# Optimization experiments

Hardware: AMD Instinct MI355X
Metric: run time of the kernel (lower is better)

## Reference

```python
import jax, jax.numpy as jnp
import numpy as np
from jax.scipy.linalg import solve_triangular

REG = 1e-6  # reg_covar added to covariance diagonal
LOG2PI = float(np.log(2.0 * np.pi))
RESP_EPS = 10.0 * float(np.finfo(np.float32).eps)


def _log_gauss(X, means, covs):
    # X: [N,D], means: [K,D], covs: [K,D,D] -> per-sample per-component log N(x|mu_k, Sigma_k): [N,K]
    K, D = means.shape
    eye = jnp.eye(D, dtype=X.dtype)
    chol = jnp.linalg.cholesky(covs + REG * eye)                      # [K,D,D]
    diff = X[None, :, :] - means[:, None, :]                          # [K,N,D]
    sol = jax.vmap(lambda L, d: solve_triangular(L, d.T, lower=True))(chol, diff)  # [K,D,N]
    maha = jnp.sum(sol * sol, axis=1)                                 # [K,N]
    logdet = jnp.sum(jnp.log(jnp.diagonal(chol, axis1=1, axis2=2)), axis=1)  # [K] = 0.5*log|Sigma|
    return (-0.5 * (D * LOG2PI + maha) - logdet[:, None]).T           # [N,K]


def _em_step(X, weights, means, covs):
    N, D = X.shape
    # E-step: responsibilities via stable logsumexp
    lp = _log_gauss(X, means, covs) + jnp.log(weights)[None, :]       # [N,K]
    log_norm = jax.scipy.special.logsumexp(lp, axis=1)                # [N]
    resp = jnp.exp(lp - log_norm[:, None])                            # [N,K]
    # M-step (MLE)
    nk = resp.sum(axis=0) + RESP_EPS                                  # [K]
    new_w = nk / N
    new_means = (resp.T @ X) / nk[:, None]                            # [K,D]
    diff = X[None, :, :] - new_means[:, None, :]                      # [K,N,D]
    new_covs = jnp.einsum('kn,knd,kne->kde', resp.T, diff, diff) / nk[:, None, None]
    new_covs = new_covs + REG * jnp.eye(D, dtype=X.dtype)
    return new_w, new_means, new_covs


def reference(X, weights, means, covariances, n_iter):
    # Normalize provided weights (uniform init in the torch module)
    w0 = weights / jnp.sum(weights)

    def step(carry, _):
        w, m, c = carry
        return _em_step(X, w, m, c), None

    (w, m, c), _ = jax.lax.scan(step, (w0, means, covariances), xs=None, length=n_iter)
    # Final per-sample log-likelihood under the fitted mixture (lower bound)
    lp = _log_gauss(X, m, c) + jnp.log(w)[None, :]
    return jax.scipy.special.logsumexp(lp, axis=1)                    # [N]


def setup_inputs() -> dict:
    key = jax.random.key(0)
    kx, km = jax.random.split(key)
    N, D, K = 100000, 32, 16
    X = jax.random.normal(kx, (N, D), dtype=jnp.float32)
    weights = jnp.ones((K,), dtype=jnp.float32) / K
    means = jax.random.normal(km, (K, D), dtype=jnp.float32)
    covariances = jnp.tile(jnp.eye(D, dtype=jnp.float32)[None], (K, 1, 1))
    return {"X": X, "weights": weights, "means": means, "covariances": covariances, "n_iter": 5}
```

## Files before the change

kernel.cpp:

```cpp
#include <hip/hip_runtime.h>
#include <math.h>

#define REGC 1e-6f
#define LOG2PI 1.83787706640934534f
#define RESP_EPS 1.1920929e-6f

#define NPART_MAX 256
#define PART_K 1156
#define PART_BLK (16 * PART_K)
#define RS 16

typedef __attribute__((ext_vector_type(8))) short short8;
typedef __attribute__((ext_vector_type(4))) float f32x4;
typedef unsigned short ushort_t;
typedef unsigned int uint_t;

__device__ __forceinline__ ushort_t f2bf(float x) {
    uint_t u = __float_as_uint(x);
    uint_t r = (u + 0x7fffu + ((u >> 16) & 1u)) >> 16;
    return (ushort_t)r;
}
__device__ __forceinline__ float bf2f(ushort_t h) {
    return __uint_as_float(((uint_t)h) << 16);
}
__device__ __forceinline__ void split2(float av, ushort_t& h, ushort_t& l) {
    uint_t u = __float_as_uint(av);
    float hf = __uint_as_float(u & 0xffff0000u);
    h = (ushort_t)(u >> 16);
    l = f2bf(av - hf);
}

__global__ void gmm_init(const float* __restrict__ w, const float* __restrict__ mu,
                         const float* __restrict__ cov, float* __restrict__ P0) {
    int t = blockIdx.x * 256 + threadIdx.x;
    if (t < 16) {
        float s = 0.f;
        for (int i = 0; i < 16; ++i) s += w[i];
        P0[t] = w[t] / s;
    } else if (t < 528) {
        P0[t] = mu[t - 16];
    } else if (t < 16912) {
        P0[t] = cov[t - 528];
    }
}

__global__ __launch_bounds__(256) void gmm_xsplit(const float* __restrict__ X,
                                                  ushort_t* __restrict__ Xh,
                                                  ushort_t* __restrict__ Xl,
                                                  ushort_t* __restrict__ XTH,
                                                  ushort_t* __restrict__ XTL,
                                                  int N) {
    int chunk = blockIdx.x;
    int t = threadIdx.x;
    __shared__ float xsh[32][33];
    int s = t >> 3, q = t & 7;
    int n = chunk * 32 + s;
    float4 v = make_float4(0.f, 0.f, 0.f, 0.f);
    if (n < N) v = ((const float4*)(X + (size_t)n * 32))[q];
    float vv[4] = { v.x, v.y, v.z, v.w };
    xsh[s][q * 4 + 0] = v.x; xsh[s][q * 4 + 1] = v.y;
    xsh[s][q * 4 + 2] = v.z; xsh[s][q * 4 + 3] = v.w;
    if (n < N) {
        ushort_t h[4], l[4];
#pragma unroll
        for (int i = 0; i < 4; ++i) {
            h[i] = f2bf(vv[i]);
            l[i] = f2bf(vv[i] - bf2f(h[i]));
        }
        size_t o = (size_t)n * 32 + q * 4;
        uint2 hp = make_uint2((uint_t)h[0] | ((uint_t)h[1] << 16),
                              (uint_t)h[2] | ((uint_t)h[3] << 16));
        uint2 lp = make_uint2((uint_t)l[0] | ((uint_t)l[1] << 16),
                              (uint_t)l[2] | ((uint_t)l[3] << 16));
        *(uint2*)(Xh + o) = hp;
        *(uint2*)(Xl + o) = lp;
    }
    __syncthreads();
    int di = t >> 7;
    int lane = (t >> 1) & 63;
    int jj0 = (t & 1) * 4;
    int c = lane & 15, quad = lane >> 4;
    int d = di * 16 + c;
    ushort_t fh[4], fl[4];
#pragma unroll
    for (int i = 0; i < 4; ++i) {
        float x = xsh[quad * 8 + jj0 + i][d];
        fh[i] = f2bf(x);
        fl[i] = f2bf(x - bf2f(fh[i]));
    }
    size_t fo = ((size_t)(chunk * 2 + di) * 64 + lane) * 8 + jj0;
    uint2 hp = make_uint2((uint_t)fh[0] | ((uint_t)fh[1] << 16),
                          (uint_t)fh[2] | ((uint_t)fh[3] << 16));
    uint2 lp = make_uint2((uint_t)fl[0] | ((uint_t)fl[1] << 16),
                          (uint_t)fl[2] | ((uint_t)fl[3] << 16));
    *(uint2*)(XTH + fo) = hp;
    *(uint2*)(XTL + fo) = lp;
}

__global__ __launch_bounds__(64) void gmm_prep(const float* __restrict__ P,
                                               ushort_t* __restrict__ Wh,
                                               ushort_t* __restrict__ Wl,
                                               float* __restrict__ Bv,
                                               float* __restrict__ Cc) {
    int k = blockIdx.x;
    int t = threadIdx.x;
    __shared__ float L[32][33];
    __shared__ float Ai[32][33];
    const float* cov = P + 528 + k * 1024;
    const float* mu  = P + 16 + k * 32;

#pragma unroll
    for (int rep = 0; rep < 16; ++rep) {
        int idx = rep * 64 + t;
        int i = idx >> 5, j = idx & 31;
        L[i][j] = cov[idx] + (i == j ? REGC : 0.f);
    }
    __syncthreads();

#pragma unroll
    for (int j = 0; j < 32; ++j) {
        float s = L[j][j];
#pragma unroll
        for (int p = 0; p < j; ++p) { float v = L[j][p]; s -= v * v; }
        float dj = sqrtf(s);
        if (t > j && t < 32) {
            float s2 = L[t][j];
#pragma unroll
            for (int p = 0; p < j; ++p) s2 -= L[t][p] * L[j][p];
            L[t][j] = s2 / dj;
        }
        if (t == j) L[j][j] = dj;
        __syncthreads();
    }

    if (t < 32) {
        float ai[32];
#pragma unroll
        for (int r = 0; r < 32; ++r) {
            float s = (r == t) ? 1.f : 0.f;
#pragma unroll
            for (int p = 0; p < r; ++p) s -= L[r][p] * ai[p];
            ai[r] = s / L[r][r];
        }
#pragma unroll
        for (int r = 0; r < 32; ++r) Ai[r][t] = ai[r];
    }
    __syncthreads();

#pragma unroll
    for (int rep = 0; rep < 16; ++rep) {
        int idx = rep * 64 + t;
        int i = idx >> 5, j = idx & 31;
        float v = Ai[i][j];
        ushort_t h = f2bf(v);
        Wh[(size_t)(k * 32 + i) * 32 + j] = h;
        Wl[(size_t)(k * 32 + i) * 32 + j] = f2bf(v - bf2f(h));
    }
    if (t < 32) {
        float s = 0.f;
#pragma unroll
        for (int j = 0; j < 32; ++j) s += Ai[t][j] * mu[j];
        Bv[k * 32 + t] = s;
    }
    float lv = (t < 32) ? logf(L[t & 31][t & 31]) : 0.f;
#pragma unroll
    for (int off = 1; off < 32; off <<= 1) lv += __shfl_xor(lv, off);
    if (t == 0) Cc[k] = logf(P[k]) - 0.5f * 32.0f * LOG2PI - lv;
}

__global__ __launch_bounds__(256, 2) void gmm_estep(const ushort_t* __restrict__ Xh,
                                                    const ushort_t* __restrict__ Xl,
                                                    const ushort_t* __restrict__ Wh,
                                                    const ushort_t* __restrict__ Wl,
                                                    const float* __restrict__ Bv,
                                                    const float* __restrict__ Cc,
                                                    float* __restrict__ resp,
                                                    float* __restrict__ out,
                                                    int N, int mode) {
    int t = threadIdx.x;
    int wave = t >> 6, lane = t & 63;
    int quad = lane >> 4, c = lane & 15;
    int base = (blockIdx.x * 4 + wave) * 16;
    if (base + 16 > N) base = (N >= 16) ? (N - 16) : 0;

    short8 ah = *(const short8*)(Xh + (size_t)(base + c) * 32 + quad * 8);
    short8 al = *(const short8*)(Xl + (size_t)(base + c) * 32 + quad * 8);

    f32x4 lpv[16];
#pragma unroll
    for (int k = 0; k < 16; ++k) {
        const size_t w0 = (size_t)(k * 32 + c) * 32 + quad * 8;
        const size_t w1 = (size_t)(k * 32 + 16 + c) * 32 + quad * 8;
        short8 bh0 = *(const short8*)(Wh + w0);
        short8 bl0 = *(const short8*)(Wl + w0);
        short8 bh1 = *(const short8*)(Wh + w1);
        short8 bl1 = *(const short8*)(Wl + w1);
        f32x4 acc0 = {0.f, 0.f, 0.f, 0.f};
        f32x4 acc1 = {0.f, 0.f, 0.f, 0.f};
        acc0 = __builtin_amdgcn_mfma_f32_16x16x32_bf16(ah, bh0, acc0, 0, 0, 0);
        acc0 = __builtin_amdgcn_mfma_f32_16x16x32_bf16(ah, bl0, acc0, 0, 0, 0);
        acc0 = __builtin_amdgcn_mfma_f32_16x16x32_bf16(al, bh0, acc0, 0, 0, 0);
        acc1 = __builtin_amdgcn_mfma_f32_16x16x32_bf16(ah, bh1, acc1, 0, 0, 0);
        acc1 = __builtin_amdgcn_mfma_f32_16x16x32_bf16(ah, bl1, acc1, 0, 0, 0);
        acc1 = __builtin_amdgcn_mfma_f32_16x16x32_bf16(al, bh1, acc1, 0, 0, 0);

        float bv0 = Bv[k * 32 + c];
        float bv1 = Bv[k * 32 + 16 + c];
        f32x4 ms;
#pragma unroll
        for (int r = 0; r < 4; ++r) {
            float d0 = acc0[r] - bv0;
            float d1 = acc1[r] - bv1;
            ms[r] = fmaf(d0, d0, d1 * d1);
        }
#pragma unroll
        for (int off = 1; off < 16; off <<= 1) {
#pragma unroll
            for (int r = 0; r < 4; ++r) ms[r] += __shfl_xor(ms[r], off);
        }
        float cc = Cc[k];
#pragma unroll
        for (int r = 0; r < 4; ++r) lpv[k][r] = cc - 0.5f * ms[r];
    }

    f32x4 mx = lpv[0];
#pragma unroll
    for (int k = 1; k < 16; ++k)
#pragma unroll
        for (int r = 0; r < 4; ++r) mx[r] = fmaxf(mx[r], lpv[k][r]);
    f32x4 sum = {0.f, 0.f, 0.f, 0.f};
#pragma unroll
    for (int k = 0; k < 16; ++k)
#pragma unroll
        for (int r = 0; r < 4; ++r) {
            lpv[k][r] = __expf(lpv[k][r] - mx[r]);
            sum[r] += lpv[k][r];
        }

    if (mode) {
        if (c == 0) {
#pragma unroll
            for (int r = 0; r < 4; ++r)
                out[base + quad * 4 + r] = mx[r] + __logf(sum[r]);
        }
    } else {
        f32x4 sel = lpv[0];
#pragma unroll
        for (int k = 1; k < 16; ++k) {
            bool m = (c == k);
#pragma unroll
            for (int r = 0; r < 4; ++r) sel[r] = m ? lpv[k][r] : sel[r];
        }
#pragma unroll
        for (int r = 0; r < 4; ++r) sel[r] /= sum[r];
        size_t off = (size_t)c * N + base + quad * 4;
        if ((N & 3) == 0) {
            *(f32x4*)(resp + off) = sel;
        } else {
#pragma unroll
            for (int r = 0; r < 4; ++r) resp[off + r] = sel[r];
        }
    }
}

__global__ __launch_bounds__(1024, 4) void gmm_moment(const ushort_t* __restrict__ XTH,
                                                      const ushort_t* __restrict__ XTL,
                                                      const float* __restrict__ resp,
                                                      float* __restrict__ part,
                                                      int N, int NC) {
    int t = threadIdx.x;
    int k = t >> 6;
    int lane = t & 63;
    int quad = lane >> 4, c = lane & 15;
    bool al4 = ((N & 3) == 0);

    f32x4 acc00 = {0.f,0.f,0.f,0.f}, acc01 = {0.f,0.f,0.f,0.f};
    f32x4 acc10 = {0.f,0.f,0.f,0.f}, acc11 = {0.f,0.f,0.f,0.f};
    float row0 = 0.f, row1 = 0.f, corner = 0.f;

#pragma unroll 1
    for (int chunk = blockIdx.x; chunk < NC; chunk += gridDim.x) {
        size_t fb = ((size_t)chunk * 2 * 64 + lane) * 8;
        short8 bh0 = *(const short8*)(XTH + fb);
        short8 bl0 = *(const short8*)(XTL + fb);
        short8 bh1 = *(const short8*)(XTH + fb + 512);
        short8 bl1 = *(const short8*)(XTL + fb + 512);

        const float* rp = resp + (size_t)k * N + (size_t)chunk * 32 + quad * 8;
        float r[8];
        if (al4) {
            float4 ra = *(const float4*)rp;
            float4 rb = *(const float4*)(rp + 4);
            r[0]=ra.x; r[1]=ra.y; r[2]=ra.z; r[3]=ra.w;
            r[4]=rb.x; r[5]=rb.y; r[6]=rb.z; r[7]=rb.w;
        } else {
#pragma unroll
            for (int j = 0; j < 8; ++j) r[j] = rp[j];
        }
        corner += ((r[0]+r[1])+(r[2]+r[3])) + ((r[4]+r[5])+(r[6]+r[7]));

        short8 ah0, al_0, ah1, al_1;
#pragma unroll
        for (int jj = 0; jj < 8; ++jj) {
            float xf = bf2f((ushort_t)bh0[jj]) + bf2f((ushort_t)bl0[jj]);
            float av = r[jj] * xf;
            ushort_t hh, ll; split2(av, hh, ll);
            ah0[jj] = (short)hh; al_0[jj] = (short)ll;
            row0 += av;
        }
#pragma unroll
        for (int jj = 0; jj < 8; ++jj) {
            float xf = bf2f((ushort_t)bh1[jj]) + bf2f((ushort_t)bl1[jj]);
            float av = r[jj] * xf;
            ushort_t hh, ll; split2(av, hh, ll);
            ah1[jj] = (short)hh; al_1[jj] = (short)ll;
            row1 += av;
        }

        acc00 = __builtin_amdgcn_mfma_f32_16x16x32_bf16(ah0, bh0, acc00, 0, 0, 0);
        acc00 = __builtin_amdgcn_mfma_f32_16x16x32_bf16(ah0, bl0, acc00, 0, 0, 0);
        acc00 = __builtin_amdgcn_mfma_f32_16x16x32_bf16(al_0, bh0, acc00, 0, 0, 0);
        acc01 = __builtin_amdgcn_mfma_f32_16x16x32_bf16(ah0, bh1, acc01, 0, 0, 0);
        acc01 = __builtin_amdgcn_mfma_f32_16x16x32_bf16(ah0, bl1, acc01, 0, 0, 0);
        acc01 = __builtin_amdgcn_mfma_f32_16x16x32_bf16(al_0, bh1, acc01, 0, 0, 0);
        acc10 = __builtin_amdgcn_mfma_f32_16x16x32_bf16(ah1, bh0, acc10, 0, 0, 0);
        acc10 = __builtin_amdgcn_mfma_f32_16x16x32_bf16(ah1, bl0, acc10, 0, 0, 0);
        acc10 = __builtin_amdgcn_mfma_f32_16x16x32_bf16(al_1, bh0, acc10, 0, 0, 0);
        acc11 = __builtin_amdgcn_mfma_f32_16x16x32_bf16(ah1, bh1, acc11, 0, 0, 0);
        acc11 = __builtin_amdgcn_mfma_f32_16x16x32_bf16(ah1, bl1, acc11, 0, 0, 0);
        acc11 = __builtin_amdgcn_mfma_f32_16x16x32_bf16(al_1, bh1, acc11, 0, 0, 0);
    }

    row0 += __shfl_xor(row0, 16);  row0 += __shfl_xor(row0, 32);
    row1 += __shfl_xor(row1, 16);  row1 += __shfl_xor(row1, 32);
    corner += __shfl_xor(corner, 16);  corner += __shfl_xor(corner, 32);

    float* pb = part + ((size_t)blockIdx.x * 16 + k) * PART_K;
#pragma unroll
    for (int r = 0; r < 4; ++r) {
        pb[(quad * 4 + r) * 34 + c]            = acc00[r];
        pb[(quad * 4 + r) * 34 + 16 + c]       = acc01[r];
        pb[(16 + quad * 4 + r) * 34 + c]       = acc10[r];
        pb[(16 + quad * 4 + r) * 34 + 16 + c]  = acc11[r];
    }
    if (quad == 0) {
        pb[32 * 34 + c]      = row0;
        pb[32 * 34 + 16 + c] = row1;
    }
    if (lane == 0) pb[32 * 34 + 32] = corner;
}

__global__ __launch_bounds__(256) void gmm_reduce1(const float* __restrict__ part,
                                                   float* __restrict__ part2,
                                                   int npart) {
    int k = blockIdx.x, g = blockIdx.y;
    int nb = (npart + RS - 1) / RS;
    int b0 = g * nb;
    int b1 = b0 + nb; if (b1 > npart) b1 = npart;
    for (int idx = threadIdx.x; idx < PART_K; idx += 256) {
        float s = 0.f;
#pragma unroll 4
        for (int b = b0; b < b1; ++b)
            s += part[((size_t)b * 16 + k) * PART_K + idx];
        part2[((size_t)g * 16 + k) * PART_K + idx] = s;
    }
}

__global__ __launch_bounds__(256) void gmm_reduce_fin(const float* __restrict__ part2,
                                                      float* __restrict__ Pn,
                                                      int N) {
    int k = blockIdx.x;
    int t = threadIdx.x;
    __shared__ float mrow[33];
    if (t < 33) {
        float s = 0.f;
#pragma unroll
        for (int b = 0; b < RS; ++b)
            s += part2[((size_t)b * 16 + k) * PART_K + 32 * 34 + t];
        mrow[t] = s;
    }
    __syncthreads();
    float nk = mrow[32] + RESP_EPS;
    float inv = 1.f / nk;
    if (blockIdx.y == 0) {
        if (t == 0) Pn[k] = nk / (float)N;
        if (t < 32) Pn[16 + k * 32 + t] = mrow[t] * inv;
    }
    int idx = blockIdx.y * 256 + t;
    int i = idx >> 5, j = idx & 31;
    float s = 0.f;
#pragma unroll
    for (int b = 0; b < RS; ++b)
        s += part2[((size_t)b * 16 + k) * PART_K + i * 34 + j];
    float c = s * inv - (mrow[i] * inv) * (mrow[j] * inv) + ((i == j) ? REGC : 0.f);
    Pn[528 + k * 1024 + idx] = c;
}

extern "C" void kernel_launch(void* const* d_in, const int* in_sizes, int n_in,
                              void* d_out, int out_size, void* d_ws, size_t ws_size,
                              hipStream_t stream) {
    const float* X   = (const float*)d_in[0];
    const float* w   = (const float*)d_in[1];
    const float* mu  = (const float*)d_in[2];
    const float* cov = (const float*)d_in[3];
    const int NITER = 5;
    int N = in_sizes[0] / 32;
    int NC = (N + 31) / 32;

    float* ws = (float*)d_ws;
    float*    P0 = ws;
    float*    P1 = ws + 16912;
    float*    Bv = ws + 33824;
    float*    Cc = ws + 34336;
    ushort_t* Wh = (ushort_t*)(ws + 34352);
    ushort_t* Wl = (ushort_t*)(ws + 42544);
    ushort_t* Xh = (ushort_t*)(ws + 50736);
    ushort_t* Xl = (ushort_t*)(ws + 50736 + (size_t)16 * N);
    size_t xt0 = 50736 + (size_t)32 * N;
    size_t SZ  = (size_t)NC * 512;
    ushort_t* XTH = (ushort_t*)(ws + xt0);
    ushort_t* XTL = (ushort_t*)(ws + xt0 + SZ);
    float*  resp = ws + xt0 + 2 * SZ;
    size_t p2base = xt0 + 2 * SZ + (size_t)16 * N;
    float*  part2 = ws + p2base;
    size_t pbase = p2base + (size_t)RS * 16 * PART_K;
    float*  part = ws + pbase;

    long long avail = (long long)(ws_size / 4) - (long long)pbase;
    int npart = (int)(avail / PART_BLK);
    if (npart > NPART_MAX) npart = NPART_MAX;
    if (npart < 1) npart = 1;

    float* out = (float*)d_out;

    int eblocks = ((N + 15) / 16 + 3) / 4;

    gmm_init<<<67, 256, 0, stream>>>(w, mu, cov, P0);
    gmm_xsplit<<<NC, 256, 0, stream>>>(X, Xh, Xl, XTH, XTL, N);

    float* Pc = P0;
    float* Pn = P1;
    for (int it = 0; it < NITER; ++it) {
        gmm_prep<<<16, 64, 0, stream>>>(Pc, Wh, Wl, Bv, Cc);
        gmm_estep<<<eblocks, 256, 0, stream>>>(Xh, Xl, Wh, Wl, Bv, Cc, resp, out, N, 0);
        gmm_moment<<<npart, 1024, 0, stream>>>(XTH, XTL, resp, part, N, NC);
        dim3 r1(16, RS);
        gmm_reduce1<<<r1, 256, 0, stream>>>(part, part2, npart);
        dim3 r2(16, 4);
        gmm_reduce_fin<<<r2, 256, 0, stream>>>(part2, Pn, N);
        float* tmp = Pc; Pc = Pn; Pn = tmp;
    }
    gmm_prep<<<16, 64, 0, stream>>>(Pc, Wh, Wl, Bv, Cc);
    gmm_estep<<<eblocks, 256, 0, stream>>>(Xh, Xl, Wh, Wl, Bv, Cc, resp, out, N, 1);
}
```

Measured before the change: 561.4 us.

## Use single-bf16 moment MFMAs, fuse final reduce with Cholesky prep, retile E-step

The moment kernel drops the low-order bf16 split of X and of resp*X. It now does one MFMA per tile instead of three and no longer writes or reads the XTL buffer, which lowers precision of the covariance accumulation. The final reduction is fused with the Cholesky/inverse prep, removing one launch per iteration and the parameter round trip through global memory. The E-step now gives each wave 32 samples and uses a transposed butterfly reduction, so after the shuffles each lane holds the Mahalanobis sum for component c. This replaces sixteen full 16-lane reductions and the 16-entry lpv register array.

```diff
diff --git a/kernel.cpp b/kernel.cpp
--- a/kernel.cpp
+++ b/kernel.cpp
@@ -23,11 +23,17 @@
 __device__ __forceinline__ float bf2f(ushort_t h) {
     return __uint_as_float(((uint_t)h) << 16);
 }
-__device__ __forceinline__ void split2(float av, ushort_t& h, ushort_t& l) {
-    uint_t u = __float_as_uint(av);
-    float hf = __uint_as_float(u & 0xffff0000u);
-    h = (ushort_t)(u >> 16);
-    l = f2bf(av - hf);
+__device__ __forceinline__ f32x4 shx4(f32x4 v, int m) {
+    f32x4 r;
+#pragma unroll
+    for (int i = 0; i < 4; ++i) r[i] = __shfl_xor(v[i], m);
+    return r;
+}
+__device__ __forceinline__ f32x4 sel4(bool s, f32x4 b, f32x4 a) {
+    f32x4 r;
+#pragma unroll
+    for (int i = 0; i < 4; ++i) r[i] = s ? b[i] : a[i];
+    return r;
 }
 
 __global__ void gmm_init(const float* __restrict__ w, const float* __restrict__ mu,
@@ -48,7 +54,6 @@
                                                   ushort_t* __restrict__ Xh,
                                                   ushort_t* __restrict__ Xl,
                                                   ushort_t* __restrict__ XTH,
-                                                  ushort_t* __restrict__ XTL,
                                                   int N) {
     int chunk = blockIdx.x;
     int t = threadIdx.x;
@@ -81,20 +86,13 @@
     int jj0 = (t & 1) * 4;
     int c = lane & 15, quad = lane >> 4;
     int d = di * 16 + c;
-    ushort_t fh[4], fl[4];
-#pragma unroll
-    for (int i = 0; i < 4; ++i) {
-        float x = xsh[quad * 8 + jj0 + i][d];
-        fh[i] = f2bf(x);
-        fl[i] = f2bf(x - bf2f(fh[i]));
-    }
+    ushort_t fh[4];
+#pragma unroll
+    for (int i = 0; i < 4; ++i) fh[i] = f2bf(xsh[quad * 8 + jj0 + i][d]);
     size_t fo = ((size_t)(chunk * 2 + di) * 64 + lane) * 8 + jj0;
     uint2 hp = make_uint2((uint_t)fh[0] | ((uint_t)fh[1] << 16),
                           (uint_t)fh[2] | ((uint_t)fh[3] << 16));
-    uint2 lp = make_uint2((uint_t)fl[0] | ((uint_t)fl[1] << 16),
-                          (uint_t)fl[2] | ((uint_t)fl[3] << 16));
     *(uint2*)(XTH + fo) = hp;
-    *(uint2*)(XTL + fo) = lp;
 }
 
 __global__ __launch_bounds__(64) void gmm_prep(const float* __restrict__ P,
@@ -180,91 +178,111 @@
     int t = threadIdx.x;
     int wave = t >> 6, lane = t & 63;
     int quad = lane >> 4, c = lane & 15;
-    int base = (blockIdx.x * 4 + wave) * 16;
-    if (base + 16 > N) base = (N >= 16) ? (N - 16) : 0;
-
-    short8 ah = *(const short8*)(Xh + (size_t)(base + c) * 32 + quad * 8);
-    short8 al = *(const short8*)(Xl + (size_t)(base + c) * 32 + quad * 8);
-
-    f32x4 lpv[16];
+    int wstart = (blockIdx.x * 4 + wave) * 32;
+    if (wstart + 32 > N) wstart = (N >= 32) ? (N - 32) : 0;
+    bool al4 = ((N & 3) == 0);
+
+    size_t xo0 = (size_t)(wstart + c) * 32 + quad * 8;
+    size_t xo1 = (size_t)(wstart + 16 + c) * 32 + quad * 8;
+    short8 ah0 = *(const short8*)(Xh + xo0);
+    short8 al0 = *(const short8*)(Xl + xo0);
+    short8 ah1 = *(const short8*)(Xh + xo1);
+    short8 al1 = *(const short8*)(Xl + xo1);
+
+    f32x4 p0[2], p1[2], p2[2], p3[2], fin[2];
+
 #pragma unroll
     for (int k = 0; k < 16; ++k) {
-        const size_t w0 = (size_t)(k * 32 + c) * 32 + quad * 8;
-        const size_t w1 = (size_t)(k * 32 + 16 + c) * 32 + quad * 8;
+        size_t w0 = (size_t)(k * 32 + c) * 32 + quad * 8;
+        size_t w1 = w0 + 512;
         short8 bh0 = *(const short8*)(Wh + w0);
         short8 bl0 = *(const short8*)(Wl + w0);
         short8 bh1 = *(const short8*)(Wh + w1);
         short8 bl1 = *(const short8*)(Wl + w1);
-        f32x4 acc0 = {0.f, 0.f, 0.f, 0.f};
-        f32x4 acc1 = {0.f, 0.f, 0.f, 0.f};
-        acc0 = __builtin_amdgcn_mfma_f32_16x16x32_bf16(ah, bh0, acc0, 0, 0, 0);
-        acc0 = __builtin_amdgcn_mfma_f32_16x16x32_bf16(ah, bl0, acc0, 0, 0, 0);
-        acc0 = __builtin_amdgcn_mfma_f32_16x16x32_bf16(al, bh0, acc0, 0, 0, 0);
-        acc1 = __builtin_amdgcn_mfma_f32_16x16x32_bf16(ah, bh1, acc1, 0, 0, 0);
-        acc1 = __builtin_amdgcn_mfma_f32_16x16x32_bf16(ah, bl1, acc1, 0, 0, 0);
-        acc1 = __builtin_amdgcn_mfma_f32_16x16x32_bf16(al, bh1, acc1, 0, 0, 0);
-
         float bv0 = Bv[k * 32 + c];
         float bv1 = Bv[k * 32 + 16 + c];
-        f32x4 ms;
-#pragma unroll
-        for (int r = 0; r < 4; ++r) {
-            float d0 = acc0[r] - bv0;
-            float d1 = acc1[r] - bv1;
-            ms[r] = fmaf(d0, d0, d1 * d1);
-        }
+#pragma unroll
+        for (int tt = 0; tt < 2; ++tt) {
+            short8 ah = tt ? ah1 : ah0;
+            short8 al = tt ? al1 : al0;
+            f32x4 a0 = {0.f, 0.f, 0.f, 0.f};
+            f32x4 a1 = {0.f, 0.f, 0.f, 0.f};
+            a0 = __builtin_amdgcn_mfma_f32_16x16x32_bf16(ah, bh0, a0, 0, 0, 0);
+            a0 = __builtin_amdgcn_mfma_f32_16x16x32_bf16(ah, bl0, a0, 0, 0, 0);
+            a0 = __builtin_amdgcn_mfma_f32_16x16x32_bf16(al, bh0, a0, 0, 0, 0);
+            a1 = __builtin_amdgcn_mfma_f32_16x16x32_bf16(ah, bh1, a1, 0, 0, 0);
+            a1 = __builtin_amdgcn_mfma_f32_16x16x32_bf16(ah, bl1, a1, 0, 0, 0);
+            a1 = __builtin_amdgcn_mfma_f32_16x16x32_bf16(al, bh1, a1, 0, 0, 0);
+            f32x4 ms;
+#pragma unroll
+            for (int r = 0; r < 4; ++r) {
+                float d0 = a0[r] - bv0;
+                float d1 = a1[r] - bv1;
+                ms[r] = fmaf(d0, d0, d1 * d1);
+            }
+            if ((k & 1) == 0) { p0[tt] = ms; }
+            else {
+                f32x4 a = p0[tt] + shx4(p0[tt], 1);
+                f32x4 b = ms + shx4(ms, 1);
+                f32x4 v = sel4((c & 1) != 0, b, a);
+                if ((k & 2) == 0) { p1[tt] = v; }
+                else {
+                    a = p1[tt] + shx4(p1[tt], 2); b = v + shx4(v, 2); v = sel4((c & 2) != 0, b, a);
+                    if ((k & 4) == 0) { p2[tt] = v; }
+                    else {
+                        a = p2[tt] + shx4(p2[tt], 4); b = v + shx4(v, 4); v = sel4((c & 4) != 0, b, a);
+                        if ((k & 8) == 0) { p3[tt] = v; }
+                        else {
+                            a = p3[tt] + shx4(p3[tt], 8); b = v + shx4(v, 8);
+                            fin[tt] = sel4((c & 8) != 0, b, a);
+                        }
+                    }
+                }
+            }
+        }
+    }
+
+    float cc = Cc[c];
+#pragma unroll
+    for (int tt = 0; tt < 2; ++tt) {
+        f32x4 lp;
+#pragma unroll
+        for (int r = 0; r < 4; ++r) lp[r] = cc - 0.5f * fin[tt][r];
+        f32x4 mx = lp;
 #pragma unroll
         for (int off = 1; off < 16; off <<= 1) {
-#pragma unroll
-            for (int r = 0; r < 4; ++r) ms[r] += __shfl_xor(ms[r], off);
-        }
-        float cc = Cc[k];
-#pragma unroll
-        for (int r = 0; r < 4; ++r) lpv[k][r] = cc - 0.5f * ms[r];
-    }
-
-    f32x4 mx = lpv[0];
-#pragma unroll
-    for (int k = 1; k < 16; ++k)
-#pragma unroll
-        for (int r = 0; r < 4; ++r) mx[r] = fmaxf(mx[r], lpv[k][r]);
-    f32x4 sum = {0.f, 0.f, 0.f, 0.f};
-#pragma unroll
-    for (int k = 0; k < 16; ++k)
-#pragma unroll
-        for (int r = 0; r < 4; ++r) {
-            lpv[k][r] = __expf(lpv[k][r] - mx[r]);
-            sum[r] += lpv[k][r];
-        }
-
-    if (mode) {
-        if (c == 0) {
-#pragma unroll
-            for (int r = 0; r < 4; ++r)
-                out[base + quad * 4 + r] = mx[r] + __logf(sum[r]);
-        }
-    } else {
-        f32x4 sel = lpv[0];
-#pragma unroll
-        for (int k = 1; k < 16; ++k) {
-            bool m = (c == k);
-#pragma unroll
-            for (int r = 0; r < 4; ++r) sel[r] = m ? lpv[k][r] : sel[r];
-        }
-#pragma unroll
-        for (int r = 0; r < 4; ++r) sel[r] /= sum[r];
-        size_t off = (size_t)c * N + base + quad * 4;
-        if ((N & 3) == 0) {
-            *(f32x4*)(resp + off) = sel;
+            f32x4 s = shx4(mx, off);
+#pragma unroll
+            for (int r = 0; r < 4; ++r) mx[r] = fmaxf(mx[r], s[r]);
+        }
+        f32x4 e;
+#pragma unroll
+        for (int r = 0; r < 4; ++r) e[r] = __expf(lp[r] - mx[r]);
+        f32x4 sm = e;
+#pragma unroll
+        for (int off = 1; off < 16; off <<= 1) sm = sm + shx4(sm, off);
+
+        int nb = wstart + tt * 16 + quad * 4;
+        if (mode) {
+            if (c == 0) {
+                f32x4 o;
+#pragma unroll
+                for (int r = 0; r < 4; ++r) o[r] = mx[r] + __logf(sm[r]);
+                if (al4) *(f32x4*)(out + nb) = o;
+                else { for (int r = 0; r < 4; ++r) out[nb + r] = o[r]; }
+            }
         } else {
-#pragma unroll
-            for (int r = 0; r < 4; ++r) resp[off + r] = sel[r];
+            f32x4 sv;
+#pragma unroll
+            for (int r = 0; r < 4; ++r) sv[r] = e[r] / sm[r];
+            size_t off = (size_t)c * N + nb;
+            if (al4) *(f32x4*)(resp + off) = sv;
+            else { for (int r = 0; r < 4; ++r) resp[off + r] = sv[r]; }
         }
     }
 }
 
 __global__ __launch_bounds__(1024, 4) void gmm_moment(const ushort_t* __restrict__ XTH,
-                                                      const ushort_t* __restrict__ XTL,
                                                       const float* __restrict__ resp,
                                                       float* __restrict__ part,
                                                       int N, int NC) {
@@ -282,9 +300,7 @@
     for (int chunk = blockIdx.x; chunk < NC; chunk += gridDim.x) {
         size_t fb = ((size_t)chunk * 2 * 64 + lane) * 8;
         short8 bh0 = *(const short8*)(XTH + fb);
-        short8 bl0 = *(const short8*)(XTL + fb);
         short8 bh1 = *(const short8*)(XTH + fb + 512);
-        short8 bl1 = *(const short8*)(XTL + fb + 512);
 
         const float* rp = resp + (size_t)k * N + (size_t)chunk * 32 + quad * 8;
         float r[8];
@@ -299,36 +315,23 @@
         }
         corner += ((r[0]+r[1])+(r[2]+r[3])) + ((r[4]+r[5])+(r[6]+r[7]));
 
-        short8 ah0, al_0, ah1, al_1;
+        short8 a0, a1;
 #pragma unroll
         for (int jj = 0; jj < 8; ++jj) {
-            float xf = bf2f((ushort_t)bh0[jj]) + bf2f((ushort_t)bl0[jj]);
-            float av = r[jj] * xf;
-            ushort_t hh, ll; split2(av, hh, ll);
-            ah0[jj] = (short)hh; al_0[jj] = (short)ll;
-            row0 += av;
-        }
-#pragma unroll
-        for (int jj = 0; jj < 8; ++jj) {
-            float xf = bf2f((ushort_t)bh1[jj]) + bf2f((ushort_t)bl1[jj]);
-            float av = r[jj] * xf;
-            ushort_t hh, ll; split2(av, hh, ll);
-            ah1[jj] = (short)hh; al_1[jj] = (short)ll;
-            row1 += av;
-        }
-
-        acc00 = __builtin_amdgcn_mfma_f32_16x16x32_bf16(ah0, bh0, acc00, 0, 0, 0);
-        acc00 = __builtin_amdgcn_mfma_f32_16x16x32_bf16(ah0, bl0, acc00, 0, 0, 0);
-        acc00 = __builtin_amdgcn_mfma_f32_16x16x32_bf16(al_0, bh0, acc00, 0, 0, 0);
-        acc01 = __builtin_amdgcn_mfma_f32_16x16x32_bf16(ah0, bh1, acc01, 0, 0, 0);
-        acc01 = __builtin_amdgcn_mfma_f32_16x16x32_bf16(ah0, bl1, acc01, 0, 0, 0);
-        acc01 = __builtin_amdgcn_mfma_f32_16x16x32_bf16(al_0, bh1, acc01, 0, 0, 0);
-        acc10 = __builtin_amdgcn_mfma_f32_16x16x32_bf16(ah1, bh0, acc10, 0, 0, 0);
-        acc10 = __builtin_amdgcn_mfma_f32_16x16x32_bf16(ah1, bl0, acc10, 0, 0, 0);
-        acc10 = __builtin_amdgcn_mfma_f32_16x16x32_bf16(al_1, bh0, acc10, 0, 0, 0);
-        acc11 = __builtin_amdgcn_mfma_f32_16x16x32_bf16(ah1, bh1, acc11, 0, 0, 0);
-        acc11 = __builtin_amdgcn_mfma_f32_16x16x32_bf16(ah1, bl1, acc11, 0, 0, 0);
-        acc11 = __builtin_amdgcn_mfma_f32_16x16x32_bf16(al_1, bh1, acc11, 0, 0, 0);
+            float x0 = bf2f((ushort_t)bh0[jj]);
+            float av0 = r[jj] * x0;
+            a0[jj] = (short)f2bf(av0);
+            row0 += av0;
+            float x1 = bf2f((ushort_t)bh1[jj]);
+            float av1 = r[jj] * x1;
+            a1[jj] = (short)f2bf(av1);
+            row1 += av1;
+        }
+
+        acc00 = __builtin_amdgcn_mfma_f32_16x16x32_bf16(a0, bh0, acc00, 0, 0, 0);
+        acc01 = __builtin_amdgcn_mfma_f32_16x16x32_bf16(a0, bh1, acc01, 0, 0, 0);
+        acc10 = __builtin_amdgcn_mfma_f32_16x16x32_bf16(a1, bh0, acc10, 0, 0, 0);
+        acc11 = __builtin_amdgcn_mfma_f32_16x16x32_bf16(a1, bh1, acc11, 0, 0, 0);
     }
 
     row0 += __shfl_xor(row0, 16);  row0 += __shfl_xor(row0, 32);
@@ -366,34 +369,87 @@
     }
 }
 
-__global__ __launch_bounds__(256) void gmm_reduce_fin(const float* __restrict__ part2,
-                                                      float* __restrict__ Pn,
-                                                      int N) {
+__global__ __launch_bounds__(256) void gmm_redfin_prep(const float* __restrict__ part2,
+                                                       ushort_t* __restrict__ Wh,
+                                                       ushort_t* __restrict__ Wl,
+                                                       float* __restrict__ Bv,
+                                                       float* __restrict__ Cc,
+                                                       int N) {
     int k = blockIdx.x;
     int t = threadIdx.x;
-    __shared__ float mrow[33];
-    if (t < 33) {
+    __shared__ float S[1156];
+    __shared__ float L[32][33];
+    __shared__ float Ai[32][33];
+
+    for (int idx = t; idx < 1156; idx += 256) {
         float s = 0.f;
 #pragma unroll
         for (int b = 0; b < RS; ++b)
-            s += part2[((size_t)b * 16 + k) * PART_K + 32 * 34 + t];
-        mrow[t] = s;
+            s += part2[((size_t)b * 16 + k) * PART_K + idx];
+        S[idx] = s;
     }
     __syncthreads();
-    float nk = mrow[32] + RESP_EPS;
+    float nk = S[32 * 34 + 32] + RESP_EPS;
     float inv = 1.f / nk;
-    if (blockIdx.y == 0) {
-        if (t == 0) Pn[k] = nk / (float)N;
-        if (t < 32) Pn[16 + k * 32 + t] = mrow[t] * inv;
-    }
-    int idx = blockIdx.y * 256 + t;
-    int i = idx >> 5, j = idx & 31;
-    float s = 0.f;
-#pragma unroll
-    for (int b = 0; b < RS; ++b)
-        s += part2[((size_t)b * 16 + k) * PART_K + i * 34 + j];
-    float c = s * inv - (mrow[i] * inv) * (mrow[j] * inv) + ((i == j) ? REGC : 0.f);
-    Pn[528 + k * 1024 + idx] = c;
+    for (int idx = t; idx < 1024; idx += 256) {
+        int i = idx >> 5, j = idx & 31;
+        float mi = S[32 * 34 + i] * inv;
+        float mj = S[32 * 34 + j] * inv;
+        L[i][j] = S[i * 34 + j] * inv - mi * mj + ((i == j) ? 2.f * REGC : 0.f);
+    }
+    __syncthreads();
+
+#pragma unroll
+    for (int j = 0; j < 32; ++j) {
+        if (t < 32) {
+            float s = L[j][j];
+#pragma unroll
+            for (int p = 0; p < j; ++p) { float v = L[j][p]; s -= v * v; }
+            float dj = sqrtf(s);
+            if (t > j) {
+                float s2 = L[t][j];
+#pragma unroll
+                for (int p = 0; p < j; ++p) s2 -= L[t][p] * L[j][p];
+                L[t][j] = s2 / dj;
+            }
+            if (t == j) L[j][j] = dj;
+        }
+        __syncthreads();
+    }
+
+    if (t < 32) {
+        float ai[32];
+#pragma unroll
+        for (int r = 0; r < 32; ++r) {
+            float s = (r == t) ? 1.f : 0.f;
+#pragma unroll
+            for (int p = 0; p < r; ++p) s -= L[r][p] * ai[p];
+            ai[r] = s / L[r][r];
+        }
+#pragma unroll
+        for (int r = 0; r < 32; ++r) Ai[r][t] = ai[r];
+    }
+    __syncthreads();
+
+#pragma unroll
+    for (int rep = 0; rep < 4; ++rep) {
+        int idx = rep * 256 + t;
+        int i = idx >> 5, j = idx & 31;
+        float v = Ai[i][j];
+        ushort_t h = f2bf(v);
+        Wh[(size_t)(k * 32 + i) * 32 + j] = h;
+        Wl[(size_t)(k * 32 + i) * 32 + j] = f2bf(v - bf2f(h));
+    }
+    if (t < 32) {
+        float s = 0.f;
+#pragma unroll
+        for (int j = 0; j < 32; ++j) s += Ai[t][j] * (S[32 * 34 + j] * inv);
+        Bv[k * 32 + t] = s;
+    }
+    float lv = (t < 32) ? logf(L[t & 31][t & 31]) : 0.f;
+#pragma unroll
+    for (int off = 1; off < 32; off <<= 1) lv += __shfl_xor(lv, off);
+    if (t == 0) Cc[k] = logf(nk / (float)N) - 0.5f * 32.0f * LOG2PI - lv;
 }
 
 extern "C" void kernel_launch(void* const* d_in, const int* in_sizes, int n_in,
@@ -409,19 +465,17 @@
 
     float* ws = (float*)d_ws;
     float*    P0 = ws;
-    float*    P1 = ws + 16912;
-    float*    Bv = ws + 33824;
-    float*    Cc = ws + 34336;
-    ushort_t* Wh = (ushort_t*)(ws + 34352);
-    ushort_t* Wl = (ushort_t*)(ws + 42544);
-    ushort_t* Xh = (ushort_t*)(ws + 50736);
-    ushort_t* Xl = (ushort_t*)(ws + 50736 + (size_t)16 * N);
-    size_t xt0 = 50736 + (size_t)32 * N;
+    float*    Bv = ws + 16912;
+    float*    Cc = ws + 17424;
+    ushort_t* Wh = (ushort_t*)(ws + 17440);
+    ushort_t* Wl = (ushort_t*)(ws + 25632);
+    ushort_t* Xh = (ushort_t*)(ws + 33824);
+    ushort_t* Xl = (ushort_t*)(ws + 33824 + (size_t)16 * N);
+    size_t xt0 = 33824 + (size_t)32 * N;
     size_t SZ  = (size_t)NC * 512;
     ushort_t* XTH = (ushort_t*)(ws + xt0);
-    ushort_t* XTL = (ushort_t*)(ws + xt0 + SZ);
-    float*  resp = ws + xt0 + 2 * SZ;
-    size_t p2base = xt0 + 2 * SZ + (size_t)16 * N;
+    float*  resp = ws + xt0 + SZ;
+    size_t p2base = xt0 + SZ + (size_t)16 * N;
     float*  part2 = ws + p2base;
     size_t pbase = p2base + (size_t)RS * 16 * PART_K;
     float*  part = ws + pbase;
@@ -433,23 +487,18 @@
 
     float* out = (float*)d_out;
 
-    int eblocks = ((N + 15) / 16 + 3) / 4;
+    int eblocks = ((N + 31) / 32 + 3) / 4;
 
     gmm_init<<<67, 256, 0, stream>>>(w, mu, cov, P0);
-    gmm_xsplit<<<NC, 256, 0, stream>>>(X, Xh, Xl, XTH, XTL, N);
-
-    float* Pc = P0;
-    float* Pn = P1;
+    gmm_xsplit<<<NC, 256, 0, stream>>>(X, Xh, Xl, XTH, N);
+    gmm_prep<<<16, 64, 0, stream>>>(P0, Wh, Wl, Bv, Cc);
+
     for (int it = 0; it < NITER; ++it) {
-        gmm_prep<<<16, 64, 0, stream>>>(Pc, Wh, Wl, Bv, Cc);
         gmm_estep<<<eblocks, 256, 0, stream>>>(Xh, Xl, Wh, Wl, Bv, Cc, resp, out, N, 0);
-        gmm_moment<<<npart, 1024, 0, stream>>>(XTH, XTL, resp, part, N, NC);
+        gmm_moment<<<npart, 1024, 0, stream>>>(XTH, resp, part, N, NC);
         dim3 r1(16, RS);
         gmm_reduce1<<<r1, 256, 0, stream>>>(part, part2, npart);
-        dim3 r2(16, 4);
-        gmm_reduce_fin<<<r2, 256, 0, stream>>>(part2, Pn, N);
-        float* tmp = Pc; Pc = Pn; Pn = tmp;
-    }
-    gmm_prep<<<16, 64, 0, stream>>>(Pc, Wh, Wl, Bv, Cc);
+        gmm_redfin_prep<<<16, 256, 0, stream>>>(part2, Wh, Wl, Bv, Cc, N);
+    }
     gmm_estep<<<eblocks, 256, 0, stream>>>(Xh, Xl, Wh, Wl, Bv, Cc, resp, out, N, 1);
 }
```

New measurement: 478.1 us. 1.17x faster.
